# Kernel optimization log

Hardware: AMD Instinct MI355X
Metric: run time of the kernel (lower is better)

The kernel has to match this reference:

```python
import jax, jax.numpy as jnp
import numpy as np

N_NODES = 50000
N_EDGES = 800000
D_IN = 128
D_HID = 128
D_OUT = 128
EPS = 0.1  # GINConv eps


def setup_inputs() -> dict:
    key = jax.random.key(0)
    k = jax.random.split(key, 8)
    scale = 1.0 / np.sqrt(D_IN)
    return {
        "x": jax.random.normal(k[0], (N_NODES, D_IN), dtype=jnp.float32),
        "edge_index": jax.random.randint(k[1], (2, N_EDGES), 0, N_NODES, dtype=jnp.int64),
        "edge_weight": jax.random.uniform(k[2], (N_EDGES,), dtype=jnp.float32),
        "W1a": jax.random.normal(k[3], (D_IN, D_HID), dtype=jnp.float32) * scale,
        "W1b": jax.random.normal(k[4], (D_HID, D_HID), dtype=jnpp.float32) if False else jax.random.normal(k[4], (D_HID, D_HID), dtype=jnp.float32) * scale,
        "W2a": jax.random.normal(k[5], (D_HID, D_HID), dtype=jnp.float32) * scale,
        "W2b": jax.random.normal(k[6], (D_HID, D_OUT), dtype=jnp.float32) * scale,
    }


def _gin_conv(h, src, dst, ew, Wa, Wb, n_nodes):
    # edge-weighted neighbor sum: aggr[i] = sum_{(j->i)} w_ji * h[j]
    msg = ew[:, None] * h[src]                       # [E, d]
    aggr = jax.ops.segment_sum(msg, dst, num_segments=n_nodes)  # [N, d]
    z = (1.0 + EPS) * h + aggr                       # GIN update
    # 2-layer bias-free MLP: lin -> relu -> lin
    return jnp.maximum(z @ Wa, 0.0) @ Wb


def reference(x, edge_index, edge_weight, W1a, W1b, W2a, W2b):
    src, dst = edge_index[0], edge_index[1]
    n = x.shape[0]
    h = _gin_conv(x, src, dst, edge_weight, W1a, W1b, n)
    h = jnp.maximum(h, 0.0)  # relu between convs; dropout is identity in eval
    h = _gin_conv(h, src, dst, edge_weight, W2a, W2b, n)
    return h
```

## Files before the change

### kernel.cpp

```cpp
#include <hip/hip_runtime.h>
#include <hip/hip_fp16.h>

#define D 128
#define N_NODES 50000
#define EPSP1 1.1f

#define NPB 128
#define NBUCK 391
#define CAP 2560
#define P1E 1024
#define TS 136
#define ECAP 1024

typedef __attribute__((ext_vector_type(8))) short short8;
typedef __attribute__((ext_vector_type(4))) float f32x4;

__device__ __forceinline__ unsigned short f2bf(float f) {
    unsigned u = __float_as_uint(f);
    u += 0x7FFF + ((u >> 16) & 1);
    return (unsigned short)(u >> 16);
}
__device__ __forceinline__ float bf2f(unsigned short h) {
    return __uint_as_float(((unsigned)h) << 16);
}

__global__ __launch_bounds__(256) void pass1_all(
    const int* __restrict__ src, const int* __restrict__ dst,
    const float* __restrict__ ew, int* __restrict__ gcnt,
    uint2* __restrict__ gstage, int ne, int nb1,
    const float* __restrict__ x, unsigned short* __restrict__ hb,
    int n4, int ncvt,
    const float* __restrict__ W1a, const float* __restrict__ W1b,
    const float* __restrict__ W2a, const float* __restrict__ W2b,
    unsigned short* __restrict__ wp)
{
    __shared__ int bcnt[NBUCK];
    __shared__ int goff[NBUCK];
    int tid = threadIdx.x;
    int bid = blockIdx.x;

    if (bid < nb1) {
        for (int i = tid; i < NBUCK; i += 256) bcnt[i] = 0;
        __syncthreads();
        int e0 = bid * P1E;
        int   rank[4];
        int   buck[4];
        uint2 pay[4];
#pragma unroll
        for (int j = 0; j < 4; ++j) {
            int e = e0 + j * 256 + tid;
            buck[j] = -1;
            if (e < ne) {
                int d_ = dst[e];
                int b  = d_ >> 7;
                int dl = d_ & 127;
                pay[j].x = (unsigned)(src[e] & 0xFFFF) | ((unsigned)dl << 16);
                pay[j].y = (unsigned)__half_as_ushort(__float2half_rn(ew[e]));
                rank[j]  = atomicAdd(&bcnt[b], 1);
                buck[j]  = b;
            }
        }
        __syncthreads();
        for (int i = tid; i < NBUCK; i += 256)
            if (bcnt[i] > 0) goff[i] = atomicAdd(&gcnt[i], bcnt[i]);
        __syncthreads();
#pragma unroll
        for (int j = 0; j < 4; ++j) {
            if (buck[j] >= 0) {
                int pos = goff[buck[j]] + rank[j];
                if (pos < CAP)
                    gstage[(size_t)buck[j] * CAP + pos] = pay[j];
            }
        }
    } else if (bid < nb1 + ncvt) {
        int base = (bid - nb1) * 2048;
#pragma unroll
        for (int it = 0; it < 8; ++it) {
            int i = base + it * 256 + tid;
            if (i < n4) {
                float4 v = ((const float4*)x)[i];
                ushort4 o;
                o.x = f2bf(v.x); o.y = f2bf(v.y); o.z = f2bf(v.z); o.w = f2bf(v.w);
                ((ushort4*)hb)[i] = o;
            }
        }
    } else {
        int e2 = (bid - nb1 - ncvt) * 256 + tid;
        if (e2 < 8192) {
            int mat = e2 >> 11;
            int e   = e2 & 2047;
            const float* W = (mat == 0) ? W1a : (mat == 1) ? W1b : (mat == 2) ? W2a : W2b;
            unsigned short* Wp = wp + (size_t)mat * 16384;
            int col = e & 127;
            int kq  = e >> 7;
            short8 v;
#pragma unroll
            for (int j = 0; j < 8; ++j)
                v[j] = (short)f2bf(W[(size_t)(kq * 8 + j) * 128 + col]);
            ((short8*)Wp)[e] = v;
        }
    }
}

__global__ __launch_bounds__(512) void csr_build(
    const uint2* __restrict__ gstage, const int* __restrict__ gcnt,
    unsigned* __restrict__ epay, int* __restrict__ off)
{
    __shared__ int hist[NPB];
    __shared__ int scn[NPB];
    __shared__ int loc[NPB];
    __shared__ int wtot[2];
    __shared__ int base_s;
    __shared__ unsigned csr[CAP];

    int b = blockIdx.x;
    int t = threadIdx.x;
    int cnt = min(gcnt[b], CAP);

    if (t < NPB) hist[t] = 0;
    __syncthreads();

    uint2 ent[CAP / 512];
#pragma unroll
    for (int it = 0; it < CAP / 512; ++it) {
        int i = it * 512 + t;
        if (i < cnt) {
            ent[it] = gstage[(size_t)b * CAP + i];
            atomicAdd(&hist[(ent[it].x >> 16) & 255], 1);
        }
    }
    __syncthreads();

    int w = t >> 6, l = t & 63;
    if (w < 2) {
        int v = hist[w * 64 + l];
#pragma unroll
        for (int dd = 1; dd < 64; dd <<= 1) {
            int u = __shfl_up(v, dd, 64);
            if (l >= dd) v += u;
        }
        scn[w * 64 + l] = v;
        if (l == 63) wtot[w] = v;
    } else if (w == 2) {
        int v = 0;
        for (int i = l; i < NBUCK; i += 64)
            if (i < b) v += min(gcnt[i], CAP);
#pragma unroll
        for (int dd = 32; dd > 0; dd >>= 1) v += __shfl_down(v, dd, 64);
        if (l == 0) base_s = v;
    }
    __syncthreads();

    if (t < NPB) {
        int pre = (t >= 64) ? wtot[0] : 0;
        int incl = scn[t] + pre;
        int excl = incl - hist[t];
        int node = (b << 7) + t;
        if (node <= N_NODES) off[node] = base_s + excl;
        loc[t] = excl;
    }
    __syncthreads();

#pragma unroll
    for (int it = 0; it < CAP / 512; ++it) {
        int i = it * 512 + t;
        if (i < cnt) {
            int dl = (ent[it].x >> 16) & 255;
            int p = atomicAdd(&loc[dl], 1);
            csr[p] = (ent[it].x & 0xFFFF) | (ent[it].y << 16);
        }
    }
    __syncthreads();

    for (int i = t; i < cnt; i += 512)
        epay[base_s + i] = csr[i];
}

template<bool L>
__device__ __forceinline__ void gather_node(
    const unsigned short* __restrict__ h,
    const unsigned* eLp, const unsigned* __restrict__ egp,
    int lb, int le, int sub, float* acc)
{
    int i = lb;
    for (; i + 4 <= le; i += 4) {
        unsigned p0 = L ? eLp[i]     : egp[i];
        unsigned p1 = L ? eLp[i + 1] : egp[i + 1];
        unsigned p2 = L ? eLp[i + 2] : egp[i + 2];
        unsigned p3 = L ? eLp[i + 3] : egp[i + 3];
        short8 v0 = ((const short8*)(h + (size_t)(p0 & 0xFFFF) * D))[sub];
        short8 v1 = ((const short8*)(h + (size_t)(p1 & 0xFFFF) * D))[sub];
        short8 v2 = ((const short8*)(h + (size_t)(p2 & 0xFFFF) * D))[sub];
        short8 v3 = ((const short8*)(h + (size_t)(p3 & 0xFFFF) * D))[sub];
        float w0 = __half2float(__ushort_as_half((unsigned short)(p0 >> 16)));
        float w1 = __half2float(__ushort_as_half((unsigned short)(p1 >> 16)));
        float w2 = __half2float(__ushort_as_half((unsigned short)(p2 >> 16)));
        float w3 = __half2float(__ushort_as_half((unsigned short)(p3 >> 16)));
#pragma unroll
        for (int c = 0; c < 8; ++c)
            acc[c] += w0 * bf2f((unsigned short)v0[c]) + w1 * bf2f((unsigned short)v1[c])
                    + w2 * bf2f((unsigned short)v2[c]) + w3 * bf2f((unsigned short)v3[c]);
    }
    for (; i < le; ++i) {
        unsigned p0 = L ? eLp[i] : egp[i];
        short8 v0 = ((const short8*)(h + (size_t)(p0 & 0xFFFF) * D))[sub];
        float w0 = __half2float(__ushort_as_half((unsigned short)(p0 >> 16)));
#pragma unroll
        for (int c = 0; c < 8; ++c)
            acc[c] += w0 * bf2f((unsigned short)v0[c]);
    }
}

template<int RELU2, int OUT_F32>
__global__ __launch_bounds__(256, 8) void conv_fused(
    const unsigned short* __restrict__ h, const int* __restrict__ off,
    const unsigned* __restrict__ epay,
    const unsigned short* __restrict__ WpA,
    const unsigned short* __restrict__ WpB,
    void* __restrict__ outv, int n)
{
    __shared__ unsigned short t1[16 * TS];
    __shared__ unsigned short t2[16 * TS];
    __shared__ unsigned eL[ECAP];
    __shared__ int offs[17];

    int tid  = threadIdx.x;
    int wave = tid >> 6;
    int lane = tid & 63;
    int qtr  = lane >> 4;
    int sub  = lane & 15;
    int nb   = blockIdx.x * 16;

    if (tid < 17) offs[tid] = off[min(nb + tid, n)];
    __syncthreads();
    int ebeg = offs[0];
    int ecnt = offs[16] - ebeg;
    int stg  = min(ecnt, ECAP);
    for (int i = tid; i < stg; i += 256) eL[i] = epay[ebeg + i];
    __syncthreads();

    int row  = wave * 4 + qtr;
    int node = nb + row;
    int lb = offs[row]     - ebeg;
    int le = offs[row + 1] - ebeg;

    float acc[8];
#pragma unroll
    for (int c = 0; c < 8; ++c) acc[c] = 0.f;

    if (ecnt <= ECAP)
        gather_node<true >(h, eL, epay + ebeg, lb, le, sub, acc);
    else
        gather_node<false>(h, eL, epay + ebeg, lb, le, sub, acc);

    {
        const short8 zero8 = {0, 0, 0, 0, 0, 0, 0, 0};
        short8 o;
        if (node < n) {
            short8 xv = ((const short8*)(h + (size_t)node * D))[sub];
#pragma unroll
            for (int c = 0; c < 8; ++c)
                o[c] = (short)f2bf(acc[c] + EPSP1 * bf2f((unsigned short)xv[c]));
        } else {
            o = zero8;
        }
        *(short8*)&t1[row * TS + sub * 8] = o;
    }
    __syncthreads();

    short8 a[4];
#pragma unroll
    for (int kk = 0; kk < 4; ++kk)
        a[kk] = *(const short8*)&t1[sub * TS + kk * 32 + qtr * 8];

    f32x4 acc2[2];
#pragma unroll
    for (int j = 0; j < 2; ++j) acc2[j] = (f32x4){0.f, 0.f, 0.f, 0.f};

#pragma unroll
    for (int j = 0; j < 2; ++j) {
        int cf = wave * 2 + j;
        short8 b[4];
#pragma unroll
        for (int kk = 0; kk < 4; ++kk)
            b[kk] = *(const short8*)(WpA + ((size_t)(kk * 4 + qtr) * 128 + cf * 16 + sub) * 8);
#pragma unroll
        for (int kk = 0; kk < 4; ++kk)
            acc2[j] = __builtin_amdgcn_mfma_f32_16x16x32_bf16(a[kk], b[kk], acc2[j], 0, 0, 0);
    }

#pragma unroll
    for (int j = 0; j < 2; ++j) {
        int cf = wave * 2 + j;
#pragma unroll
        for (int reg = 0; reg < 4; ++reg) {
            int r = qtr * 4 + reg;
            t2[r * TS + cf * 16 + sub] = f2bf(fmaxf(acc2[j][reg], 0.f));
        }
    }
    __syncthreads();

#pragma unroll
    for (int kk = 0; kk < 4; ++kk)
        a[kk] = *(const short8*)&t2[sub * TS + kk * 32 + qtr * 8];

#pragma unroll
    for (int j = 0; j < 2; ++j) acc2[j] = (f32x4){0.f, 0.f, 0.f, 0.f};

#pragma unroll
    for (int j = 0; j < 2; ++j) {
        int cf = wave * 2 + j;
        short8 b[4];
#pragma unroll
        for (int kk = 0; kk < 4; ++kk)
            b[kk] = *(const short8*)(WpB + ((size_t)(kk * 4 + qtr) * 128 + cf * 16 + sub) * 8);
#pragma unroll
        for (int kk = 0; kk < 4; ++kk)
            acc2[j] = __builtin_amdgcn_mfma_f32_16x16x32_bf16(a[kk], b[kk], acc2[j], 0, 0, 0);
    }

#pragma unroll
    for (int j = 0; j < 2; ++j) {
        int cf = wave * 2 + j;
#pragma unroll
        for (int reg = 0; reg < 4; ++reg) {
            int r = nb + qtr * 4 + reg;
            if (r < n) {
                float v = acc2[j][reg];
                if (RELU2) v = fmaxf(v, 0.f);
                int col = cf * 16 + sub;
                if (OUT_F32)
                    ((float*)outv)[(size_t)r * D + col] = v;
                else
                    ((unsigned short*)outv)[(size_t)r * D + col] = f2bf(v);
            }
        }
    }
}

extern "C" void kernel_launch(void* const* d_in, const int* in_sizes, int n_in,
                              void* d_out, int out_size, void* d_ws, size_t ws_size,
                              hipStream_t stream) {
    const float* x   = (const float*)d_in[0];
    const int*   ei  = (const int*)d_in[1];
    const float* ew  = (const float*)d_in[2];
    const float* W1a = (const float*)d_in[3];
    const float* W1b = (const float*)d_in[4];
    const float* W2a = (const float*)d_in[5];
    const float* W2b = (const float*)d_in[6];
    float* out = (float*)d_out;

    int n_edges = in_sizes[2];
    const int* src = ei;
    const int* dst = ei + n_edges;

    size_t node_elems = (size_t)N_NODES * D;
    unsigned short* hb = (unsigned short*)d_ws;
    unsigned short* zb = hb + node_elems;
    unsigned short* wp = zb + node_elems;
    unsigned* epay = (unsigned*)(wp + 4 * 16384);
    uint2*  gstage = (uint2*)(epay + n_edges);
    int*    gcnt   = (int*)(gstage + (size_t)NBUCK * CAP);
    int*    off    = gcnt + NBUCK;

    int nb1   = (n_edges + P1E - 1) / P1E;
    int n4    = (int)(node_elems / 4);
    int ncvt  = (n4 + 2047) / 2048;
    int npack = 32;
    int cgrid = (N_NODES + 15) / 16;

    hipMemsetAsync(gcnt, 0, NBUCK * sizeof(int), stream);

    pass1_all<<<nb1 + ncvt + npack, 256, 0, stream>>>(
        src, dst, ew, gcnt, gstage, n_edges, nb1,
        x, hb, n4, ncvt, W1a, W1b, W2a, W2b, wp);

    csr_build<<<NBUCK, 512, 0, stream>>>(gstage, gcnt, epay, off);

    unsigned short* wp0 = wp;
    unsigned short* wp1 = wp + 16384;
    unsigned short* wp2 = wp + 2 * 16384;
    unsigned short* wp3 = wp + 3 * 16384;

    conv_fused<1, 0><<<cgrid, 256, 0, stream>>>(hb, off, epay, wp0, wp1, zb, N_NODES);

    conv_fused<0, 1><<<cgrid, 256, 0, stream>>>(zb, off, epay, wp2, wp3, out, N_NODES);
}
```

Measured before the change: 190.6 us.

## Enlarge conv blocks to 32 nodes, share weight fragments, drop LDS edge staging

The fused GIN conv kernel now processes 32 nodes per 512-thread block. Each wave owns one output column tile and reuses its weight fragment across two 16-row MFMA tiles, which halves weight loads per node. The shared-memory staging of edge payloads is removed, so the gather reads the CSR directly from global memory. The preprocessing kernel also moves to 512 threads with 4096 edges per block, giving fewer blocks and fewer global bucket atomics, at the cost of more registers per thread.

```diff
diff --git a/kernel.cpp b/kernel.cpp
--- a/kernel.cpp
+++ b/kernel.cpp
@@ -8,9 +8,8 @@
 #define NPB 128
 #define NBUCK 391
 #define CAP 2560
-#define P1E 1024
+#define P1E 4096
 #define TS 136
-#define ECAP 1024
 
 typedef __attribute__((ext_vector_type(8))) short short8;
 typedef __attribute__((ext_vector_type(4))) float f32x4;
@@ -24,7 +23,7 @@
     return __uint_as_float(((unsigned)h) << 16);
 }
 
-__global__ __launch_bounds__(256) void pass1_all(
+__global__ __launch_bounds__(512, 4) void pass1_all(
     const int* __restrict__ src, const int* __restrict__ dst,
     const float* __restrict__ ew, int* __restrict__ gcnt,
     uint2* __restrict__ gstage, int ne, int nb1,
@@ -40,15 +39,15 @@
     int bid = blockIdx.x;
 
     if (bid < nb1) {
-        for (int i = tid; i < NBUCK; i += 256) bcnt[i] = 0;
+        for (int i = tid; i < NBUCK; i += 512) bcnt[i] = 0;
         __syncthreads();
         int e0 = bid * P1E;
-        int   rank[4];
-        int   buck[4];
-        uint2 pay[4];
-#pragma unroll
-        for (int j = 0; j < 4; ++j) {
-            int e = e0 + j * 256 + tid;
+        int   rank[8];
+        int   buck[8];
+        uint2 pay[8];
+#pragma unroll
+        for (int j = 0; j < 8; ++j) {
+            int e = e0 + j * 512 + tid;
             buck[j] = -1;
             if (e < ne) {
                 int d_ = dst[e];
@@ -61,11 +60,11 @@
             }
         }
         __syncthreads();
-        for (int i = tid; i < NBUCK; i += 256)
+        for (int i = tid; i < NBUCK; i += 512)
             if (bcnt[i] > 0) goff[i] = atomicAdd(&gcnt[i], bcnt[i]);
         __syncthreads();
 #pragma unroll
-        for (int j = 0; j < 4; ++j) {
+        for (int j = 0; j < 8; ++j) {
             if (buck[j] >= 0) {
                 int pos = goff[buck[j]] + rank[j];
                 if (pos < CAP)
@@ -73,10 +72,10 @@
             }
         }
     } else if (bid < nb1 + ncvt) {
-        int base = (bid - nb1) * 2048;
+        int base = (bid - nb1) * 4096;
 #pragma unroll
         for (int it = 0; it < 8; ++it) {
-            int i = base + it * 256 + tid;
+            int i = base + it * 512 + tid;
             if (i < n4) {
                 float4 v = ((const float4*)x)[i];
                 ushort4 o;
@@ -85,7 +84,7 @@
             }
         }
     } else {
-        int e2 = (bid - nb1 - ncvt) * 256 + tid;
+        int e2 = (bid - nb1 - ncvt) * 512 + tid;
         if (e2 < 8192) {
             int mat = e2 >> 11;
             int e   = e2 & 2047;
@@ -176,18 +175,43 @@
         epay[base_s + i] = csr[i];
 }
 
-template<bool L>
-__device__ __forceinline__ void gather_node(
-    const unsigned short* __restrict__ h,
-    const unsigned* eLp, const unsigned* __restrict__ egp,
-    int lb, int le, int sub, float* acc)
+template<int RELU2, int OUT_F32>
+__global__ __launch_bounds__(512, 8) void conv_fused(
+    const unsigned short* __restrict__ h, const int* __restrict__ off,
+    const unsigned* __restrict__ epay,
+    const unsigned short* __restrict__ WpA,
+    const unsigned short* __restrict__ WpB,
+    void* __restrict__ outv, int n)
 {
-    int i = lb;
-    for (; i + 4 <= le; i += 4) {
-        unsigned p0 = L ? eLp[i]     : egp[i];
-        unsigned p1 = L ? eLp[i + 1] : egp[i + 1];
-        unsigned p2 = L ? eLp[i + 2] : egp[i + 2];
-        unsigned p3 = L ? eLp[i + 3] : egp[i + 3];
+    __shared__ unsigned short t1[32 * TS];
+    __shared__ unsigned short t2[32 * TS];
+    __shared__ int offs[33];
+
+    int tid  = threadIdx.x;
+    int wave = tid >> 6;
+    int lane = tid & 63;
+    int qtr  = lane >> 4;
+    int sub  = lane & 15;
+    int nb   = blockIdx.x * 32;
+
+    if (tid < 33) offs[tid] = off[min(nb + tid, n)];
+    __syncthreads();
+
+    int row  = wave * 4 + qtr;
+    int node = nb + row;
+    int beg = offs[row];
+    int end = offs[row + 1];
+
+    float acc[8];
+#pragma unroll
+    for (int c = 0; c < 8; ++c) acc[c] = 0.f;
+
+    int i = beg;
+    for (; i + 4 <= end; i += 4) {
+        unsigned p0 = epay[i];
+        unsigned p1 = epay[i + 1];
+        unsigned p2 = epay[i + 2];
+        unsigned p3 = epay[i + 3];
         short8 v0 = ((const short8*)(h + (size_t)(p0 & 0xFFFF) * D))[sub];
         short8 v1 = ((const short8*)(h + (size_t)(p1 & 0xFFFF) * D))[sub];
         short8 v2 = ((const short8*)(h + (size_t)(p2 & 0xFFFF) * D))[sub];
@@ -201,57 +225,14 @@
             acc[c] += w0 * bf2f((unsigned short)v0[c]) + w1 * bf2f((unsigned short)v1[c])
                     + w2 * bf2f((unsigned short)v2[c]) + w3 * bf2f((unsigned short)v3[c]);
     }
-    for (; i < le; ++i) {
-        unsigned p0 = L ? eLp[i] : egp[i];
+    for (; i < end; ++i) {
+        unsigned p0 = epay[i];
         short8 v0 = ((const short8*)(h + (size_t)(p0 & 0xFFFF) * D))[sub];
         float w0 = __half2float(__ushort_as_half((unsigned short)(p0 >> 16)));
 #pragma unroll
         for (int c = 0; c < 8; ++c)
             acc[c] += w0 * bf2f((unsigned short)v0[c]);
     }
-}
-
-template<int RELU2, int OUT_F32>
-__global__ __launch_bounds__(256, 8) void conv_fused(
-    const unsigned short* __restrict__ h, const int* __restrict__ off,
-    const unsigned* __restrict__ epay,
-    const unsigned short* __restrict__ WpA,
-    const unsigned short* __restrict__ WpB,
-    void* __restrict__ outv, int n)
-{
-    __shared__ unsigned short t1[16 * TS];
-    __shared__ unsigned short t2[16 * TS];
-    __shared__ unsigned eL[ECAP];
-    __shared__ int offs[17];
-
-    int tid  = threadIdx.x;
-    int wave = tid >> 6;
-    int lane = tid & 63;
-    int qtr  = lane >> 4;
-    int sub  = lane & 15;
-    int nb   = blockIdx.x * 16;
-
-    if (tid < 17) offs[tid] = off[min(nb + tid, n)];
-    __syncthreads();
-    int ebeg = offs[0];
-    int ecnt = offs[16] - ebeg;
-    int stg  = min(ecnt, ECAP);
-    for (int i = tid; i < stg; i += 256) eL[i] = epay[ebeg + i];
-    __syncthreads();
-
-    int row  = wave * 4 + qtr;
-    int node = nb + row;
-    int lb = offs[row]     - ebeg;
-    int le = offs[row + 1] - ebeg;
-
-    float acc[8];
-#pragma unroll
-    for (int c = 0; c < 8; ++c) acc[c] = 0.f;
-
-    if (ecnt <= ECAP)
-        gather_node<true >(h, eL, epay + ebeg, lb, le, sub, acc);
-    else
-        gather_node<false>(h, eL, epay + ebeg, lb, le, sub, acc);
 
     {
         const short8 zero8 = {0, 0, 0, 0, 0, 0, 0, 0};
@@ -268,65 +249,48 @@
     }
     __syncthreads();
 
-    short8 a[4];
-#pragma unroll
-    for (int kk = 0; kk < 4; ++kk)
-        a[kk] = *(const short8*)&t1[sub * TS + kk * 32 + qtr * 8];
-
+    int cf = wave;
     f32x4 acc2[2];
-#pragma unroll
-    for (int j = 0; j < 2; ++j) acc2[j] = (f32x4){0.f, 0.f, 0.f, 0.f};
-
-#pragma unroll
-    for (int j = 0; j < 2; ++j) {
-        int cf = wave * 2 + j;
-        short8 b[4];
-#pragma unroll
-        for (int kk = 0; kk < 4; ++kk)
-            b[kk] = *(const short8*)(WpA + ((size_t)(kk * 4 + qtr) * 128 + cf * 16 + sub) * 8);
-#pragma unroll
-        for (int kk = 0; kk < 4; ++kk)
-            acc2[j] = __builtin_amdgcn_mfma_f32_16x16x32_bf16(a[kk], b[kk], acc2[j], 0, 0, 0);
-    }
-
-#pragma unroll
-    for (int j = 0; j < 2; ++j) {
-        int cf = wave * 2 + j;
+    acc2[0] = (f32x4){0.f, 0.f, 0.f, 0.f};
+    acc2[1] = (f32x4){0.f, 0.f, 0.f, 0.f};
+
+#pragma unroll
+    for (int kk = 0; kk < 4; ++kk) {
+        short8 a0 = *(const short8*)&t1[(sub)      * TS + kk * 32 + qtr * 8];
+        short8 a1 = *(const short8*)&t1[(16 + sub) * TS + kk * 32 + qtr * 8];
+        short8 b  = *(const short8*)(WpA + ((size_t)(kk * 4 + qtr) * 128 + cf * 16 + sub) * 8);
+        acc2[0] = __builtin_amdgcn_mfma_f32_16x16x32_bf16(a0, b, acc2[0], 0, 0, 0);
+        acc2[1] = __builtin_amdgcn_mfma_f32_16x16x32_bf16(a1, b, acc2[1], 0, 0, 0);
+    }
+
+#pragma unroll
+    for (int s = 0; s < 2; ++s)
 #pragma unroll
         for (int reg = 0; reg < 4; ++reg) {
-            int r = qtr * 4 + reg;
-            t2[r * TS + cf * 16 + sub] = f2bf(fmaxf(acc2[j][reg], 0.f));
-        }
-    }
-    __syncthreads();
-
-#pragma unroll
-    for (int kk = 0; kk < 4; ++kk)
-        a[kk] = *(const short8*)&t2[sub * TS + kk * 32 + qtr * 8];
-
-#pragma unroll
-    for (int j = 0; j < 2; ++j) acc2[j] = (f32x4){0.f, 0.f, 0.f, 0.f};
-
-#pragma unroll
-    for (int j = 0; j < 2; ++j) {
-        int cf = wave * 2 + j;
-        short8 b[4];
-#pragma unroll
-        for (int kk = 0; kk < 4; ++kk)
-            b[kk] = *(const short8*)(WpB + ((size_t)(kk * 4 + qtr) * 128 + cf * 16 + sub) * 8);
-#pragma unroll
-        for (int kk = 0; kk < 4; ++kk)
-            acc2[j] = __builtin_amdgcn_mfma_f32_16x16x32_bf16(a[kk], b[kk], acc2[j], 0, 0, 0);
-    }
-
-#pragma unroll
-    for (int j = 0; j < 2; ++j) {
-        int cf = wave * 2 + j;
+            int r = s * 16 + qtr * 4 + reg;
+            t2[r * TS + cf * 16 + sub] = f2bf(fmaxf(acc2[s][reg], 0.f));
+        }
+    __syncthreads();
+
+    acc2[0] = (f32x4){0.f, 0.f, 0.f, 0.f};
+    acc2[1] = (f32x4){0.f, 0.f, 0.f, 0.f};
+
+#pragma unroll
+    for (int kk = 0; kk < 4; ++kk) {
+        short8 a0 = *(const short8*)&t2[(sub)      * TS + kk * 32 + qtr * 8];
+        short8 a1 = *(const short8*)&t2[(16 + sub) * TS + kk * 32 + qtr * 8];
+        short8 b  = *(const short8*)(WpB + ((size_t)(kk * 4 + qtr) * 128 + cf * 16 + sub) * 8);
+        acc2[0] = __builtin_amdgcn_mfma_f32_16x16x32_bf16(a0, b, acc2[0], 0, 0, 0);
+        acc2[1] = __builtin_amdgcn_mfma_f32_16x16x32_bf16(a1, b, acc2[1], 0, 0, 0);
+    }
+
+#pragma unroll
+    for (int s = 0; s < 2; ++s)
 #pragma unroll
         for (int reg = 0; reg < 4; ++reg) {
-            int r = nb + qtr * 4 + reg;
+            int r = nb + s * 16 + qtr * 4 + reg;
             if (r < n) {
-                float v = acc2[j][reg];
+                float v = acc2[s][reg];
                 if (RELU2) v = fmaxf(v, 0.f);
                 int col = cf * 16 + sub;
                 if (OUT_F32)
@@ -335,7 +299,6 @@
                     ((unsigned short*)outv)[(size_t)r * D + col] = f2bf(v);
             }
         }
-    }
 }
 
 extern "C" void kernel_launch(void* const* d_in, const int* in_sizes, int n_in,
@@ -365,13 +328,13 @@
 
     int nb1   = (n_edges + P1E - 1) / P1E;
     int n4    = (int)(node_elems / 4);
-    int ncvt  = (n4 + 2047) / 2048;
-    int npack = 32;
-    int cgrid = (N_NODES + 15) / 16;
+    int ncvt  = (n4 + 4095) / 4096;
+    int npack = 16;
+    int cgrid = (N_NODES + 31) / 32;
 
     hipMemsetAsync(gcnt, 0, NBUCK * sizeof(int), stream);
 
-    pass1_all<<<nb1 + ncvt + npack, 256, 0, stream>>>(
+    pass1_all<<<nb1 + ncvt + npack, 512, 0, stream>>>(
         src, dst, ew, gcnt, gstage, n_edges, nb1,
         x, hb, n4, ncvt, W1a, W1b, W2a, W2b, wp);
 
@@ -382,7 +345,7 @@
     unsigned short* wp2 = wp + 2 * 16384;
     unsigned short* wp3 = wp + 3 * 16384;
 
-    conv_fused<1, 0><<<cgrid, 256, 0, stream>>>(hb, off, epay, wp0, wp1, zb, N_NODES);
-
-    conv_fused<0, 1><<<cgrid, 256, 0, stream>>>(zb, off, epay, wp2, wp3, out, N_NODES);
-}
+    conv_fused<1, 0><<<cgrid, 512, 0, stream>>>(hb, off, epay, wp0, wp1, zb, N_NODES);
+
+    conv_fused<0, 1><<<cgrid, 512, 0, stream>>>(zb, off, epay, wp2, wp3, out, N_NODES);
+}
```

After: 177.9 us. 1.07x faster.
